# Performance work log

Measured on AMD Instinct MI355X. Metric: run time of the kernel, lower is better.

## Reference

```python
import jax, jax.numpy as jnp
import numpy as np

N_NODES = 50000
N_EDGES = 1600000
IN_FEATS = 256
OUT_FEATS = 64


def setup_inputs() -> dict:
    key = jax.random.key(0)
    k_x, k_w, k_b, k_s, k_d = jax.random.split(key, 5)
    x = jax.random.normal(k_x, (N_NODES, IN_FEATS), dtype=jnp.float32)
    # nn.Linear(in_feats, out_feats): weight [out, in], bias [out]
    W = jax.random.normal(k_w, (OUT_FEATS, IN_FEATS), dtype=jnp.float32) / np.sqrt(IN_FEATS)
    b = jax.random.normal(k_b, (OUT_FEATS,), dtype=jnp.float32) * 0.01
    edge_src = jax.random.randint(k_s, (N_EDGES,), 0, N_NODES, dtype=jnp.int32)
    edge_dst = jax.random.randint(k_d, (N_EDGES,), 0, N_NODES, dtype=jnp.int32)
    return {"x": x, "W": W, "b": b, "edge_src": edge_src, "edge_dst": edge_dst}


def reference(x, W, b, edge_src, edge_dst):
    # h = dropout(relu(Linear(x)))  -- dropout p=0 (eval) => identity
    h = jax.nn.relu(x @ W.T + b)                     # [N, out_feats]
    # update_all: message = h[src], reduce = mean over incoming edges per dst
    msg = h[edge_src]                                # [E, out_feats] gather
    summed = jax.ops.segment_sum(msg, edge_dst, num_segments=N_NODES)  # [N, out]
    deg = jax.ops.segment_sum(jnp.ones((edge_src.shape[0],), dtype=h.dtype),
                              edge_dst, num_segments=N_NODES)          # [N]
    deg = jnp.maximum(deg, 1.0)
    return summed / deg[:, None]
```

## Files before the change

### kernel.cpp

```cpp
#include <hip/hip_runtime.h>
#include <hip/hip_bf16.h>

#define K_IN 256
#define O_OUT 64
#define NBINS 1024
#define NPB 49
#define CAP 1824
#define PART_CHUNK 4096
#define SCAN_STRIDE 1026

typedef __attribute__((ext_vector_type(8))) short short8;
typedef __attribute__((ext_vector_type(4))) float f32x4;
typedef __attribute__((ext_vector_type(2))) unsigned u32x2;

#define GLOAD2(dst, base, voff)                                          \
  asm volatile("global_load_dwordx2 %0, %1, %2"                          \
               : "=v"(dst) : "v"(voff), "s"(base))
__device__ inline void vmwait0() {
  asm volatile("s_waitcnt vmcnt(0)" ::: "memory");
  __builtin_amdgcn_sched_barrier(0);
}

__device__ inline unsigned short bf16bits(float a) {
  __hip_bfloat16 t = __float2bfloat16(a);
  return *(unsigned short*)&t;
}

__device__ inline short8 cvt8(float4 f0, float4 f1) {
  short8 r;
  r[0] = (short)bf16bits(f0.x); r[1] = (short)bf16bits(f0.y);
  r[2] = (short)bf16bits(f0.z); r[3] = (short)bf16bits(f0.w);
  r[4] = (short)bf16bits(f1.x); r[5] = (short)bf16bits(f1.y);
  r[6] = (short)bf16bits(f1.z); r[7] = (short)bf16bits(f1.w);
  return r;
}

struct GemmSmem {
  unsigned short wsb[64 * 256];
};
struct PartSmem {
  int cnt[NBINS];
  int scanb[NBINS];
  int wsum[4];
  unsigned ord[PART_CHUNK];
};
union FusedSmem {
  GemmSmem g;
  PartSmem p;
};

__device__ void gemm_body(GemmSmem& sm, int gid, const float* __restrict__ x,
                          const float* __restrict__ W,
                          const float* __restrict__ bias,
                          __hip_bfloat16* __restrict__ h, int N) {
  const int tid = threadIdx.x;
  const int lane = tid & 63;
  const int wv = tid >> 6;
  const int n0 = gid * 64;

  {
#pragma unroll
    for (int r = 0; r < 8; ++r) {
      int c = r * 256 + tid;
      const float4* ps = (const float4*)(W + c * 8);
      float4 f0 = ps[0];
      float4 f1 = ps[1];
      int row = c >> 5;
      int c16 = c & 31;
      unsigned byte = (unsigned)(row * 512 + c16 * 16);
      byte ^= (unsigned)((row & 7) << 4);
      *(short8*)((char*)sm.wsb + byte) = cvt8(f0, f1);
    }
  }
  __syncthreads();

  int anode = n0 + wv * 16 + (lane & 15);
  if (anode > N - 1) anode = N - 1;
  const float* aptr = x + (size_t)anode * K_IN + (lane >> 4) * 8;

  const int brow0 = lane & 15;
  const unsigned kb = (unsigned)((lane >> 4) * 16);
  const unsigned bswz = (unsigned)((brow0 & 7) << 4);

  f32x4 acc[4] = {{0.f, 0.f, 0.f, 0.f}, {0.f, 0.f, 0.f, 0.f},
                  {0.f, 0.f, 0.f, 0.f}, {0.f, 0.f, 0.f, 0.f}};
#pragma unroll
  for (int k8 = 0; k8 < 8; ++k8) {
    float4 f0 = *(const float4*)(aptr + k8 * 32);
    float4 f1 = *(const float4*)(aptr + k8 * 32 + 4);
    short8 a = cvt8(f0, f1);
#pragma unroll
    for (int nt = 0; nt < 4; ++nt) {
      unsigned byte = (unsigned)((brow0 + nt * 16) * 512 + k8 * 64) + kb;
      byte ^= bswz;
      short8 bfr = *(const short8*)((const char*)sm.wsb + byte);
      acc[nt] = __builtin_amdgcn_mfma_f32_16x16x32_bf16(a, bfr, acc[nt], 0, 0, 0);
    }
  }

  const int col = lane & 15;
  const int rbase = (lane >> 4) * 4;
#pragma unroll
  for (int nt = 0; nt < 4; ++nt) {
    float bv = bias[nt * 16 + col];
#pragma unroll
    for (int j = 0; j < 4; ++j) {
      int node = n0 + wv * 16 + rbase + j;
      if (node < N) {
        float v = fmaxf(acc[nt][j] + bv, 0.f);
        h[(size_t)node * O_OUT + nt * 16 + col] = __float2bfloat16(v);
      }
    }
  }
}

__device__ void part_body(PartSmem& sm, int pid, const int* __restrict__ esrc,
                          const int* __restrict__ edst,
                          unsigned* __restrict__ bucket_det,
                          unsigned short* __restrict__ scan_tab, int E) {
  const int tid = threadIdx.x;
  const int lane = tid & 63;
  const int wid = tid >> 6;
  const int base = pid * PART_CHUNK;

#pragma unroll
  for (int r = 0; r < 4; ++r) sm.cnt[r * 256 + tid] = 0;

  int4 s4[4], d4[4];
#pragma unroll
  for (int r = 0; r < 4; ++r) {
    int e0 = base + r * 1024 + tid * 4;
    if (e0 + 3 < E) {
      s4[r] = *(const int4*)(esrc + e0);
      d4[r] = *(const int4*)(edst + e0);
    } else {
      s4[r] = make_int4(0, 0, 0, 0);
      d4[r] = make_int4(0, 0, 0, 0);
      int* sp = (int*)&s4[r];
      int* dp = (int*)&d4[r];
      for (int j = 0; j < 4; ++j)
        if (e0 + j < E) { sp[j] = esrc[e0 + j]; dp[j] = edst[e0 + j]; }
    }
  }
  __syncthreads();

  unsigned pk[16];
  int rk[16];
#pragma unroll
  for (int r = 0; r < 4; ++r) {
    const int* sp = (const int*)&s4[r];
    const int* dp = (const int*)&d4[r];
#pragma unroll
    for (int j = 0; j < 4; ++j) {
      int k = r * 4 + j;
      int e = base + r * 1024 + tid * 4 + j;
      if (e < E) {
        int d = dp[j];
        int bb = (int)__umulhi((unsigned)d, 87652394u);
        int dl = d - bb * NPB;
        pk[k] = ((unsigned)sp[j] & 0xFFFFu) | ((unsigned)dl << 16) |
                ((unsigned)bb << 22);
        rk[k] = atomicAdd(&sm.cnt[bb], 1);
      } else {
        rk[k] = -1;
      }
    }
  }
  __syncthreads();

  int c0 = sm.cnt[4 * tid];
  int c1 = sm.cnt[4 * tid + 1];
  int c2 = sm.cnt[4 * tid + 2];
  int c3 = sm.cnt[4 * tid + 3];
  int s = c0 + c1 + c2 + c3;
  int incl = s;
#pragma unroll
  for (int off = 1; off < 64; off <<= 1) {
    int t = __shfl_up(incl, off);
    if (lane >= off) incl += t;
  }
  if (lane == 63) sm.wsum[wid] = incl;
  __syncthreads();
  int wpre = 0;
  for (int w = 0; w < wid; ++w) wpre += sm.wsum[w];
  int excl = wpre + incl - s;
  sm.scanb[4 * tid] = excl;
  sm.scanb[4 * tid + 1] = excl + c0;
  sm.scanb[4 * tid + 2] = excl + c0 + c1;
  sm.scanb[4 * tid + 3] = excl + c0 + c1 + c2;
  __syncthreads();

#pragma unroll
  for (int k = 0; k < 16; ++k) {
    if (rk[k] >= 0) {
      int bb = (int)(pk[k] >> 22);
      sm.ord[sm.scanb[bb] + rk[k]] = pk[k];
    }
  }
  __syncthreads();

  int nv = E - base;
  if (nv > PART_CHUNK) nv = PART_CHUNK;

  unsigned* dstp = bucket_det + (size_t)pid * PART_CHUNK;
  for (int p = tid; p < nv; p += 256) dstp[p] = sm.ord[p];
  unsigned short* st = scan_tab + (size_t)pid * SCAN_STRIDE;
  for (int i = tid; i < NBINS; i += 256) st[i] = (unsigned short)sm.scanb[i];
  if (tid == 0) st[NBINS] = (unsigned short)nv;
}

__global__ __launch_bounds__(256, 4) void k_fused(const float* __restrict__ x,
                                                  const float* __restrict__ W,
                                                  const float* __restrict__ bias,
                                                  __hip_bfloat16* __restrict__ h,
                                                  const int* __restrict__ esrc,
                                                  const int* __restrict__ edst,
                                                  unsigned* __restrict__ bucket_det,
                                                  unsigned short* __restrict__ scan_tab,
                                                  int N, int E) {
  __shared__ FusedSmem sm;
  const int npart = (E + PART_CHUNK - 1) / PART_CHUNK;
  const int b = blockIdx.x;
  if (b % 3 == 1 && b / 3 < npart) {
    part_body(sm.p, b / 3, esrc, edst, bucket_det, scan_tab, E);
  } else {
    int skipped = (b + 2) / 3;
    if (skipped > npart) skipped = npart;
    gemm_body(sm.g, b - skipped, x, W, bias, h, N);
  }
}

__global__ __launch_bounds__(256, 4) void k_sortagg(const unsigned* __restrict__ bucket_det,
                                                    const unsigned short* __restrict__ scan_tab,
                                                    const unsigned* __restrict__ h32,
                                                    float* __restrict__ out,
                                                    int N, int npart) {
  __shared__ unsigned ord32[CAP];
  __shared__ int segbase;
  __shared__ int hist[NPB];
  __shared__ int offs[NPB];
  __shared__ unsigned short sbuf[CAP + 64];

  const int tid = threadIdx.x;
  const int lane = tid & 63;
  const int wid = tid >> 6;
  const int bin = blockIdx.x;

  if (tid == 0) segbase = 0;
  if (tid < NPB) hist[tid] = 0;
  __syncthreads();

#pragma unroll
  for (int r = 0; r < 2; ++r) {
    int p = r * 256 + tid;
    int cnt_p = 0, s = 0;
    if (p < npart) {
      const unsigned short* st = scan_tab + (size_t)p * SCAN_STRIDE;
      s = st[bin];
      int e = st[bin + 1];
      cnt_p = e - s;
    }
    int incl = cnt_p;
#pragma unroll
    for (int off = 1; off < 64; off <<= 1) {
      int t = __shfl_up(incl, off);
      if (lane >= off) incl += t;
    }
    int base_w = 0;
    if (lane == 63) base_w = atomicAdd(&segbase, incl);
    base_w = __shfl(base_w, 63);
    int myofs = base_w + incl - cnt_p;
    const unsigned* srcp = bucket_det + (size_t)p * PART_CHUNK + s;
    for (int j = 0; j < cnt_p; ++j)
      if (myofs + j < CAP) ord32[myofs + j] = srcp[j];
  }
  __syncthreads();

  int cnt = segbase;
  if (cnt > CAP) cnt = CAP;

  unsigned pk2[2][4];
  int rk2[2][4];
#pragma unroll
  for (int g = 0; g < 2; ++g) {
#pragma unroll
    for (int j = 0; j < 4; ++j) {
      int i = (g * 256 + tid) * 4 + j;
      if (i < cnt) {
        unsigned w = ord32[i];
        pk2[g][j] = w;
        rk2[g][j] = atomicAdd(&hist[(w >> 16) & 63], 1);
      } else {
        rk2[g][j] = -1;
      }
    }
  }
  __syncthreads();

  if (tid < 64) {
    int hval = (tid < NPB) ? hist[tid] : 0;
    int incl = hval;
#pragma unroll
    for (int off = 1; off < 64; off <<= 1) {
      int t = __shfl_up(incl, off);
      if (lane >= off) incl += t;
    }
    if (tid < NPB) offs[tid] = incl - hval;
  }
  __syncthreads();

#pragma unroll
  for (int g = 0; g < 2; ++g)
#pragma unroll
    for (int j = 0; j < 4; ++j)
      if (rk2[g][j] >= 0)
        sbuf[offs[(pk2[g][j] >> 16) & 63] + rk2[g][j]] =
            (unsigned short)(pk2[g][j] & 0xFFFFu);
  __syncthreads();

  const int q = lane >> 4;
  const int hl = lane & 15;
  const unsigned hlb = (unsigned)hl * 8u;

  for (int nl = wid; nl < NPB; nl += 8) {
    const int nlb = nl + 4;
    const bool hasb = (nlb < NPB);
    const int ca = hist[nl];
    const int cb = hasb ? hist[nlb] : 0;
    const unsigned short* bsa = sbuf + offs[nl];
    const unsigned short* bsb = sbuf + (hasb ? offs[nlb] : 0);

    unsigned voa[12], vob[12];
#pragma unroll
    for (int k = 0; k < 12; ++k) {
      int e = k * 4 + q;
      unsigned pa = (e < ca) ? (unsigned)bsa[e] : 0u;
      unsigned pb = (e < cb) ? (unsigned)bsb[e] : 0u;
      voa[k] = pa * 128u + hlb;
      vob[k] = pb * 128u + hlb;
    }
    u32x2 ua[12], ub[12];
#pragma unroll
    for (int k = 0; k < 12; ++k) { GLOAD2(ua[k], h32, voa[k]); }
#pragma unroll
    for (int k = 0; k < 12; ++k) { GLOAD2(ub[k], h32, vob[k]); }
    vmwait0();

    float a0 = 0.f, a1 = 0.f, a2 = 0.f, a3 = 0.f;
    float b0 = 0.f, b1 = 0.f, b2 = 0.f, b3 = 0.f;
#pragma unroll
    for (int k = 0; k < 12; ++k) {
      float wk = (k * 4 + q < ca) ? 1.f : 0.f;
      a0 = fmaf(wk, __uint_as_float(ua[k][0] << 16), a0);
      a1 = fmaf(wk, __uint_as_float(ua[k][0] & 0xFFFF0000u), a1);
      a2 = fmaf(wk, __uint_as_float(ua[k][1] << 16), a2);
      a3 = fmaf(wk, __uint_as_float(ua[k][1] & 0xFFFF0000u), a3);
    }
#pragma unroll
    for (int k = 0; k < 12; ++k) {
      float wk = (k * 4 + q < cb) ? 1.f : 0.f;
      b0 = fmaf(wk, __uint_as_float(ub[k][0] << 16), b0);
      b1 = fmaf(wk, __uint_as_float(ub[k][0] & 0xFFFF0000u), b1);
      b2 = fmaf(wk, __uint_as_float(ub[k][1] << 16), b2);
      b3 = fmaf(wk, __uint_as_float(ub[k][1] & 0xFFFF0000u), b3);
    }

    const uint2* __restrict__ h2 = (const uint2*)h32;
    for (int e0 = 48; e0 < ca; e0 += 4) {
      int e = e0 + q;
      float wk = (e < ca) ? 1.f : 0.f;
      int p = (e < ca) ? (int)bsa[e] : 0;
      uint2 u = h2[(size_t)p * 16 + hl];
      a0 = fmaf(wk, __uint_as_float(u.x << 16), a0);
      a1 = fmaf(wk, __uint_as_float(u.x & 0xFFFF0000u), a1);
      a2 = fmaf(wk, __uint_as_float(u.y << 16), a2);
      a3 = fmaf(wk, __uint_as_float(u.y & 0xFFFF0000u), a3);
    }
    for (int e0 = 48; e0 < cb; e0 += 4) {
      int e = e0 + q;
      float wk = (e < cb) ? 1.f : 0.f;
      int p = (e < cb) ? (int)bsb[e] : 0;
      uint2 u = h2[(size_t)p * 16 + hl];
      b0 = fmaf(wk, __uint_as_float(u.x << 16), b0);
      b1 = fmaf(wk, __uint_as_float(u.x & 0xFFFF0000u), b1);
      b2 = fmaf(wk, __uint_as_float(u.y << 16), b2);
      b3 = fmaf(wk, __uint_as_float(u.y & 0xFFFF0000u), b3);
    }

    a0 += __shfl_xor(a0, 16); a1 += __shfl_xor(a1, 16);
    a2 += __shfl_xor(a2, 16); a3 += __shfl_xor(a3, 16);
    b0 += __shfl_xor(b0, 16); b1 += __shfl_xor(b1, 16);
    b2 += __shfl_xor(b2, 16); b3 += __shfl_xor(b3, 16);
    a0 += __shfl_xor(a0, 32); a1 += __shfl_xor(a1, 32);
    a2 += __shfl_xor(a2, 32); a3 += __shfl_xor(a3, 32);
    b0 += __shfl_xor(b0, 32); b1 += __shfl_xor(b1, 32);
    b2 += __shfl_xor(b2, 32); b3 += __shfl_xor(b3, 32);

    if (lane < 16) {
      int na = bin * NPB + nl;
      if (na < N) {
        float inv = 1.f / fmaxf((float)ca, 1.f);
        float4 r;
        r.x = a0 * inv; r.y = a1 * inv; r.z = a2 * inv; r.w = a3 * inv;
        *(float4*)(out + (size_t)na * O_OUT + hl * 4) = r;
      }
      int nb = bin * NPB + nlb;
      if (hasb && nb < N) {
        float inv = 1.f / fmaxf((float)cb, 1.f);
        float4 r;
        r.x = b0 * inv; r.y = b1 * inv; r.z = b2 * inv; r.w = b3 * inv;
        *(float4*)(out + (size_t)nb * O_OUT + hl * 4) = r;
      }
    }
  }
}

extern "C" void kernel_launch(void* const* d_in, const int* in_sizes, int n_in,
                              void* d_out, int out_size, void* d_ws, size_t ws_size,
                              hipStream_t stream) {
  const float* x = (const float*)d_in[0];
  const float* W = (const float*)d_in[1];
  const float* b = (const float*)d_in[2];
  const int* esrc = (const int*)d_in[3];
  const int* edst = (const int*)d_in[4];
  float* out = (float*)d_out;

  const int N = in_sizes[0] / K_IN;
  const int E = in_sizes[3];
  const int npart = (E + PART_CHUNK - 1) / PART_CHUNK;
  const int ngemm = (N + 63) / 64;

  char* ws = (char*)d_ws;
  __hip_bfloat16* h = (__hip_bfloat16*)ws;
  size_t off = (size_t)N * O_OUT * sizeof(__hip_bfloat16);
  unsigned* bucket_det = (unsigned*)(ws + off);
  off += (size_t)npart * PART_CHUNK * sizeof(unsigned);
  unsigned short* scan_tab = (unsigned short*)(ws + off);

  k_fused<<<ngemm + npart, 256, 0, stream>>>(x, W, b, h, esrc, edst,
                                             bucket_det, scan_tab, N, E);
  k_sortagg<<<NBINS, 256, 0, stream>>>(bucket_det, scan_tab, (const unsigned*)h,
                                       out, N, npart);
}
```

Baseline: 151.0 us.

## Merge four bins per sort-aggregate block with 512 threads

The sort-aggregate kernel now handles four consecutive bins per block using 512 threads. Each partition's contiguous range for the four bins is copied in one pass with a block-wide scan, and the histogram is built over 196 node slots. This cuts the number of scan-table reads and per-block setup, and fetches longer runs per partition. In exchange the kernel runs only 256 blocks with one block per CU, which may leave CUs idle and reduce latency hiding for the gather phase. It also relies on the 512-thread block covering every partition (one partition per thread) and on bits 22-23 of the packed word encoding the bin within the group.

```diff
diff --git a/kernel.cpp b/kernel.cpp
--- a/kernel.cpp
+++ b/kernel.cpp
@@ -8,6 +8,9 @@
 #define CAP 1824
 #define PART_CHUNK 4096
 #define SCAN_STRIDE 1026
+#define BPB 4
+#define NPG (NPB * BPB)
+#define CAP4 7168
 
 typedef __attribute__((ext_vector_type(8))) short short8;
 typedef __attribute__((ext_vector_type(4))) float f32x4;
@@ -230,66 +233,84 @@
   }
 }
 
-__global__ __launch_bounds__(256, 4) void k_sortagg(const unsigned* __restrict__ bucket_det,
+__global__ __launch_bounds__(512, 1) void k_sortagg(const unsigned* __restrict__ bucket_det,
                                                     const unsigned short* __restrict__ scan_tab,
                                                     const unsigned* __restrict__ h32,
                                                     float* __restrict__ out,
                                                     int N, int npart) {
-  __shared__ unsigned ord32[CAP];
-  __shared__ int segbase;
-  __shared__ int hist[NPB];
-  __shared__ int offs[NPB];
-  __shared__ unsigned short sbuf[CAP + 64];
+  __shared__ unsigned ord32[CAP4];
+  __shared__ unsigned short sbuf[CAP4 + 64];
+  __shared__ int hist[NPG];
+  __shared__ int offs[NPG];
+  __shared__ int wsum8[8];
 
   const int tid = threadIdx.x;
   const int lane = tid & 63;
   const int wid = tid >> 6;
-  const int bin = blockIdx.x;
-
-  if (tid == 0) segbase = 0;
-  if (tid < NPB) hist[tid] = 0;
-  __syncthreads();
-
-#pragma unroll
-  for (int r = 0; r < 2; ++r) {
-    int p = r * 256 + tid;
-    int cnt_p = 0, s = 0;
-    if (p < npart) {
-      const unsigned short* st = scan_tab + (size_t)p * SCAN_STRIDE;
-      s = st[bin];
-      int e = st[bin + 1];
-      cnt_p = e - s;
-    }
-    int incl = cnt_p;
-#pragma unroll
-    for (int off = 1; off < 64; off <<= 1) {
-      int t = __shfl_up(incl, off);
-      if (lane >= off) incl += t;
-    }
-    int base_w = 0;
-    if (lane == 63) base_w = atomicAdd(&segbase, incl);
-    base_w = __shfl(base_w, 63);
-    int myofs = base_w + incl - cnt_p;
-    const unsigned* srcp = bucket_det + (size_t)p * PART_CHUNK + s;
-    for (int j = 0; j < cnt_p; ++j)
-      if (myofs + j < CAP) ord32[myofs + j] = srcp[j];
-  }
-  __syncthreads();
-
-  int cnt = segbase;
-  if (cnt > CAP) cnt = CAP;
-
-  unsigned pk2[2][4];
-  int rk2[2][4];
-#pragma unroll
-  for (int g = 0; g < 2; ++g) {
+  const int bg = blockIdx.x;
+  const int b0 = bg * BPB;
+
+  if (tid < NPG) hist[tid] = 0;
+
+  int cnt_p = 0, s0 = 0;
+  if (tid < npart) {
+    const unsigned short* st = scan_tab + (size_t)tid * SCAN_STRIDE;
+    s0 = st[b0];
+    cnt_p = (int)st[b0 + BPB] - s0;
+  }
+  int incl = cnt_p;
+#pragma unroll
+  for (int off = 1; off < 64; off <<= 1) {
+    int t = __shfl_up(incl, off);
+    if (lane >= off) incl += t;
+  }
+  if (lane == 63) wsum8[wid] = incl;
+  __syncthreads();
+  int wpre = 0, total = 0;
+#pragma unroll
+  for (int w = 0; w < 8; ++w) {
+    int v = wsum8[w];
+    if (w < wid) wpre += v;
+    total += v;
+  }
+  int myofs = wpre + incl - cnt_p;
+  {
+    const unsigned* srcp = bucket_det + (size_t)tid * PART_CHUNK + s0;
+    int j = 0;
+    for (; j + 4 <= cnt_p; j += 4) {
+      unsigned v0 = srcp[j], v1 = srcp[j + 1], v2 = srcp[j + 2], v3 = srcp[j + 3];
+      int d = myofs + j;
+      if (d + 3 < CAP4) {
+        ord32[d] = v0; ord32[d + 1] = v1; ord32[d + 2] = v2; ord32[d + 3] = v3;
+      } else {
+        if (d < CAP4) ord32[d] = v0;
+        if (d + 1 < CAP4) ord32[d + 1] = v1;
+        if (d + 2 < CAP4) ord32[d + 2] = v2;
+        if (d + 3 < CAP4) ord32[d + 3] = v3;
+      }
+    }
+    for (; j < cnt_p; ++j) {
+      int d = myofs + j;
+      if (d < CAP4) ord32[d] = srcp[j];
+    }
+  }
+  __syncthreads();
+
+  int cnt = total;
+  if (cnt > CAP4) cnt = CAP4;
+
+  unsigned pk2[4][4];
+  int rk2[4][4];
+#pragma unroll
+  for (int g = 0; g < 4; ++g) {
 #pragma unroll
     for (int j = 0; j < 4; ++j) {
-      int i = (g * 256 + tid) * 4 + j;
+      int i = g * 2048 + tid * 4 + j;
       if (i < cnt) {
         unsigned w = ord32[i];
         pk2[g][j] = w;
-        rk2[g][j] = atomicAdd(&hist[(w >> 16) & 63], 1);
+        int gidx = (int)((w >> 22) & 3u) * NPB + (int)((w >> 16) & 63u);
+        rk2[g][j] = atomicAdd(&hist[gidx], 1);
       } else {
         rk2[g][j] = -1;
       }
@@ -298,37 +319,46 @@
   __syncthreads();
 
   if (tid < 64) {
-    int hval = (tid < NPB) ? hist[tid] : 0;
-    int incl = hval;
+    int c0 = (4 * tid < NPG) ? hist[4 * tid] : 0;
+    int c1 = (4 * tid + 1 < NPG) ? hist[4 * tid + 1] : 0;
+    int c2 = (4 * tid + 2 < NPG) ? hist[4 * tid + 2] : 0;
+    int c3 = (4 * tid + 3 < NPG) ? hist[4 * tid + 3] : 0;
+    int s = c0 + c1 + c2 + c3;
+    int inc = s;
 #pragma unroll
     for (int off = 1; off < 64; off <<= 1) {
-      int t = __shfl_up(incl, off);
-      if (lane >= off) incl += t;
-    }
-    if (tid < NPB) offs[tid] = incl - hval;
-  }
-  __syncthreads();
-
-#pragma unroll
-  for (int g = 0; g < 2; ++g)
+      int t = __shfl_up(inc, off);
+      if (lane >= off) inc += t;
+    }
+    int excl = inc - s;
+    if (4 * tid < NPG) offs[4 * tid] = excl;
+    if (4 * tid + 1 < NPG) offs[4 * tid + 1] = excl + c0;
+    if (4 * tid + 2 < NPG) offs[4 * tid + 2] = excl + c0 + c1;
+    if (4 * tid + 3 < NPG) offs[4 * tid + 3] = excl + c0 + c1 + c2;
+  }
+  __syncthreads();
+
+#pragma unroll
+  for (int g = 0; g < 4; ++g)
 #pragma unroll
     for (int j = 0; j < 4; ++j)
-      if (rk2[g][j] >= 0)
-        sbuf[offs[(pk2[g][j] >> 16) & 63] + rk2[g][j]] =
-            (unsigned short)(pk2[g][j] & 0xFFFFu);
+      if (rk2[g][j] >= 0) {
+        unsigned w = pk2[g][j];
+        int gidx = (int)((w >> 22) & 3u) * NPB + (int)((w >> 16) & 63u);
+        sbuf[offs[gidx] + rk2[g][j]] = (unsigned short)(w & 0xFFFFu);
+      }
   __syncthreads();
 
   const int q = lane >> 4;
   const int hl = lane & 15;
   const unsigned hlb = (unsigned)hl * 8u;
 
-  for (int nl = wid; nl < NPB; nl += 8) {
-    const int nlb = nl + 4;
-    const bool hasb = (nlb < NPB);
-    const int ca = hist[nl];
-    const int cb = hasb ? hist[nlb] : 0;
-    const unsigned short* bsa = sbuf + offs[nl];
-    const unsigned short* bsb = sbuf + (hasb ? offs[nlb] : 0);
+  for (int gA = wid; gA < NPG / 2; gA += 8) {
+    const int gB = gA + NPG / 2;
+    const int ca = hist[gA];
+    const int cb = hist[gB];
+    const unsigned short* bsa = sbuf + offs[gA];
+    const unsigned short* bsb = sbuf + offs[gB];
 
     unsigned voa[12], vob[12];
 #pragma unroll
@@ -347,7 +377,7 @@
     vmwait0();
 
     float a0 = 0.f, a1 = 0.f, a2 = 0.f, a3 = 0.f;
-    float b0 = 0.f, b1 = 0.f, b2 = 0.f, b3 = 0.f;
+    float b0f = 0.f, b1 = 0.f, b2 = 0.f, b3 = 0.f;
 #pragma unroll
     for (int k = 0; k < 12; ++k) {
       float wk = (k * 4 + q < ca) ? 1.f : 0.f;
@@ -359,7 +389,7 @@
 #pragma unroll
     for (int k = 0; k < 12; ++k) {
       float wk = (k * 4 + q < cb) ? 1.f : 0.f;
-      b0 = fmaf(wk, __uint_as_float(ub[k][0] << 16), b0);
+      b0f = fmaf(wk, __uint_as_float(ub[k][0] << 16), b0f);
       b1 = fmaf(wk, __uint_as_float(ub[k][0] & 0xFFFF0000u), b1);
       b2 = fmaf(wk, __uint_as_float(ub[k][1] << 16), b2);
       b3 = fmaf(wk, __uint_as_float(ub[k][1] & 0xFFFF0000u), b3);
@@ -381,7 +411,7 @@
       float wk = (e < cb) ? 1.f : 0.f;
       int p = (e < cb) ? (int)bsb[e] : 0;
       uint2 u = h2[(size_t)p * 16 + hl];
-      b0 = fmaf(wk, __uint_as_float(u.x << 16), b0);
+      b0f = fmaf(wk, __uint_as_float(u.x << 16), b0f);
       b1 = fmaf(wk, __uint_as_float(u.x & 0xFFFF0000u), b1);
       b2 = fmaf(wk, __uint_as_float(u.y << 16), b2);
       b3 = fmaf(wk, __uint_as_float(u.y & 0xFFFF0000u), b3);
@@ -389,26 +419,26 @@
 
     a0 += __shfl_xor(a0, 16); a1 += __shfl_xor(a1, 16);
     a2 += __shfl_xor(a2, 16); a3 += __shfl_xor(a3, 16);
-    b0 += __shfl_xor(b0, 16); b1 += __shfl_xor(b1, 16);
+    b0f += __shfl_xor(b0f, 16); b1 += __shfl_xor(b1, 16);
     b2 += __shfl_xor(b2, 16); b3 += __shfl_xor(b3, 16);
     a0 += __shfl_xor(a0, 32); a1 += __shfl_xor(a1, 32);
     a2 += __shfl_xor(a2, 32); a3 += __shfl_xor(a3, 32);
-    b0 += __shfl_xor(b0, 32); b1 += __shfl_xor(b1, 32);
+    b0f += __shfl_xor(b0f, 32); b1 += __shfl_xor(b1, 32);
     b2 += __shfl_xor(b2, 32); b3 += __shfl_xor(b3, 32);
 
     if (lane < 16) {
-      int na = bin * NPB + nl;
+      int na = bg * NPG + gA;
       if (na < N) {
         float inv = 1.f / fmaxf((float)ca, 1.f);
         float4 r;
         r.x = a0 * inv; r.y = a1 * inv; r.z = a2 * inv; r.w = a3 * inv;
         *(float4*)(out + (size_t)na * O_OUT + hl * 4) = r;
       }
-      int nb = bin * NPB + nlb;
-      if (hasb && nb < N) {
+      int nb = bg * NPG + gB;
+      if (nb < N) {
         float inv = 1.f / fmaxf((float)cb, 1.f);
         float4 r;
-        r.x = b0 * inv; r.y = b1 * inv; r.z = b2 * inv; r.w = b3 * inv;
+        r.x = b0f * inv; r.y = b1 * inv; r.z = b2 * inv; r.w = b3 * inv;
         *(float4*)(out + (size_t)nb * O_OUT + hl * 4) = r;
       }
     }
@@ -439,6 +469,6 @@
 
   k_fused<<<ngemm + npart, 256, 0, stream>>>(x, W, b, h, esrc, edst,
                                              bucket_det, scan_tab, N, E);
-  k_sortagg<<<NBINS, 256, 0, stream>>>(bucket_det, scan_tab, (const unsigned*)h,
-                                       out, N, npart);
-}
+  k_sortagg<<<NBINS / BPB, 512, 0, stream>>>(bucket_det, scan_tab,
+                                             (const unsigned*)h, out, N, npart);
+}
```

Result: no change. 149.8 us (-0.8%).
